# Kernel optimization log

Measured on AMD Instinct MI355X. Metric: run time of the kernel, lower is better.

The kernel has to match this reference:

```python
import jax, jax.numpy as jnp
import numpy as np

EPS_BN = 1e-5
EPS_LN = 1e-5


def conv2d(x, w, stride=1, padding=0):
    # x: [B,C,H,W], w: [O,I,kh,kw]
    return jax.lax.conv_general_dilated(
        x, w, (stride, stride), [(padding, padding), (padding, padding)],
        dimension_numbers=("NCHW", "OIHW", "NCHW"))


def bn_relu(x, g, b, m, v):
    inv = g / jnp.sqrt(v + EPS_BN)
    return jax.nn.relu(x * inv[None, :, None, None] + (b - m * inv)[None, :, None, None])


def haar_dwt(x):
    # orthonormal 2D Haar: [B,C,H,W] -> [B,4C,H/2,W/2] as concat(LL,LH,HL,HH)
    B, C, H, W = x.shape
    x = x.reshape(B, C, H // 2, 2, W // 2, 2)
    a = x[:, :, :, 0, :, 0]; b = x[:, :, :, 0, :, 1]
    c = x[:, :, :, 1, :, 0]; d = x[:, :, :, 1, :, 1]
    ll = (a + b + c + d) * 0.5
    lh = (a - b + c - d) * 0.5
    hl = (a + b - c - d) * 0.5
    hh = (a - b - c + d) * 0.5
    return jnp.concatenate([ll, lh, hl, hh], axis=1)


def haar_idwt(co):
    # exact inverse of haar_dwt: [B,4C,h,w] -> [B,C,2h,2w]
    B, C4, h, w = co.shape
    ll, lh, hl, hh = jnp.split(co, 4, axis=1)
    a = (ll + lh + hl + hh) * 0.5
    b = (ll - lh + hl - hh) * 0.5
    c = (ll + lh - hl - hh) * 0.5
    d = (ll - lh - hl + hh) * 0.5
    row0 = jnp.stack([a, b], axis=-1)  # [B,C,h,w,2]
    row1 = jnp.stack([c, d], axis=-1)
    y = jnp.stack([row0, row1], axis=3)  # [B,C,h,2,w,2]
    return y.reshape(B, C4 // 4, 2 * h, 2 * w)


def layernorm(x, g, b):
    mu = jnp.mean(x, axis=-1, keepdims=True)
    var = jnp.mean(jnp.square(x - mu), axis=-1, keepdims=True)
    return (x - mu) * jax.lax.rsqrt(var + EPS_LN) * g + b


def setup_inputs() -> dict:
    key = jax.random.key(0)
    ks = jax.random.split(key, 20)
    B, N, C = 16, 3136, 256
    red = C // 4  # 64
    sr = 2
    d = {}
    d["x"] = jax.random.normal(ks[0], (B, N, C), jnp.float32)
    d["height"] = 56
    d["width"] = 56
    # reduce: conv1x1 C->red (no bias) + BN
    d["reduce_w"] = jax.random.normal(ks[1], (red, C, 1, 1), jnp.float32) * 0.05
    d["bn1_g"] = jax.random.uniform(ks[2], (red,), jnp.float32, 0.5, 1.5)
    d["bn1_b"] = jax.random.normal(ks[3], (red,), jnp.float32) * 0.1
    d["bn1_m"] = jax.random.normal(ks[4], (red,), jnp.float32) * 0.1
    d["bn1_v"] = jax.random.uniform(ks[5], (red,), jnp.float32, 0.5, 1.5)
    # filter: conv3x3 C->C (no bias) + BN  (acts on 4*red = C coeff channels)
    d["filt_w"] = jax.random.normal(ks[6], (C, C, 3, 3), jnp.float32) * 0.02
    d["bn2_g"] = jax.random.uniform(ks[7], (C,), jnp.float32, 0.5, 1.5)
    d["bn2_b"] = jax.random.normal(ks[8], (C,), jnp.float32) * 0.1
    d["bn2_m"] = jax.random.normal(ks[9], (C,), jnp.float32) * 0.1
    d["bn2_v"] = jax.random.uniform(ks[10], (C,), jnp.float32, 0.5, 1.5)
    # kv_embed: conv kxk stride sr, C->C, with bias
    d["kve_w"] = jax.random.normal(ks[11], (C, C, sr, sr), jnp.float32) * 0.05
    d["kve_b"] = jnp.zeros((C,), jnp.float32)
    # q linear
    d["q_w"] = jax.random.normal(ks[12], (C, C), jnp.float32) * 0.05
    d["q_b"] = jnp.zeros((C,), jnp.float32)
    # kv layernorm + kv linear
    d["kvn_g"] = jnp.ones((C,), jnp.float32)
    d["kvn_b"] = jnp.zeros((C,), jnp.float32)
    d["kv_w"] = jax.random.normal(ks[13], (2 * C, C), jnp.float32) * 0.05
    d["kv_b"] = jnp.zeros((2 * C,), jnp.float32)
    # proj: (C + red) -> C
    d["proj_w"] = jax.random.normal(ks[14], (C, C + red), jnp.float32) * 0.05
    d["proj_b"] = jnp.zeros((C,), jnp.float32)
    return d


def reference(x, q_w, q_b, reduce_w, bn1_g, bn1_b, bn1_m, bn1_v,
              filt_w, bn2_g, bn2_b, bn2_m, bn2_v, kve_w, kve_b,
              kvn_g, kvn_b, kv_w, kv_b, proj_w, proj_b, height, width):
    B, N, C = x.shape
    H_heads, sr = 8, 2
    hd = C // H_heads
    scale = hd ** -0.5

    # queries [B,h,N,hd]
    q = (x @ q_w.T + q_b).reshape(B, N, H_heads, hd).transpose(0, 2, 1, 3)

    # spatial path
    spatial = x.transpose(0, 2, 1).reshape(B, C, height, width)
    reduced = bn_relu(conv2d(spatial, reduce_w), bn1_g, bn1_b, bn1_m, bn1_v)  # [B,C/4,H,W]
    coeffs = haar_dwt(reduced)  # [B,C,H/2,W/2]
    coeffs = bn_relu(conv2d(coeffs, filt_w, padding=1), bn2_g, bn2_b, bn2_m, bn2_v)
    local_context = haar_idwt(coeffs)  # [B,C/4,H,W]
    local_context = local_context.reshape(B, C // 4, N).transpose(0, 2, 1)  # [B,N,C/4]

    # kv path
    kv_src = conv2d(coeffs, kve_w, stride=sr) + kve_b[None, :, None, None]
    Bk, Ck, hk, wk = kv_src.shape
    kv_src = kv_src.reshape(B, C, hk * wk).transpose(0, 2, 1)  # [B,M,C]
    kv_src = layernorm(kv_src, kvn_g, kvn_b)
    kv = (kv_src @ kv_w.T + kv_b).reshape(B, -1, 2, H_heads, hd)
    kv = kv.transpose(2, 0, 3, 1, 4)  # [2,B,h,M,hd]
    key, value = kv[0], kv[1]

    # attention
    scores = jnp.einsum("bhnd,bhmd->bhnm", q, key) * scale
    probs = jax.nn.softmax(scores, axis=-1)
    attended = jnp.einsum("bhnm,bhmd->bhnd", probs, value)
    attended = attended.transpose(0, 2, 1, 3).reshape(B, N, C)

    out = jnp.concatenate([attended, local_context], axis=-1) @ proj_w.T + proj_b
    return out
```

## Files before the change

### kernel.cpp

```cpp
#include <hip/hip_runtime.h>
#include <hip/hip_bf16.h>
#include <math.h>


#define B_   16
#define NSP  3136
#define KVL  196
#define HD   32
#define LSTR 40

typedef short bf16x8 __attribute__((ext_vector_type(8)));
typedef float f32x4  __attribute__((ext_vector_type(4)));

__device__ inline unsigned int f2bf(float f) {
    unsigned int u = __float_as_uint(f);
    u += 0x7FFFu + ((u >> 16) & 1u);
    return u >> 16;
}
__device__ inline float bf2f(unsigned short u) {
    return __uint_as_float(((unsigned int)u) << 16);
}
__device__ inline f32x4 max4(f32x4 a, f32x4 b) {
    f32x4 r;
    r[0] = fmaxf(a[0], b[0]); r[1] = fmaxf(a[1], b[1]);
    r[2] = fmaxf(a[2], b[2]); r[3] = fmaxf(a[3], b[3]);
    return r;
}

__global__ __launch_bounds__(256) void wall_k(
    const float* __restrict__ q, const float* __restrict__ red,
    const float* __restrict__ kv, const float* __restrict__ proj,
    const float* __restrict__ kve, const float* __restrict__ filt,
    unsigned short* __restrict__ wpl, unsigned short* __restrict__ wkve,
    unsigned short* __restrict__ wfilt)
{
    const int bid = blockIdx.x;
    if (bid < 288) {
        const int i = bid * 256 + threadIdx.x;
        const int e = i * 4;
        const float* src; int off;
        if (e < 65536)       { src = q;    off = e; }
        else if (e < 81920)  { src = red;  off = e - 65536; }
        else if (e < 212992) { src = kv;   off = e - 81920; }
        else                 { src = proj; off = e - 212992; }
        const float4 v = *(const float4*)(src + off);
        const unsigned int p0 = f2bf(v.x) | (f2bf(v.y) << 16);
        const unsigned int p1 = f2bf(v.z) | (f2bf(v.w) << 16);
        *(uint2*)(wpl + e) = make_uint2(p0, p1);
    } else if (bid < 544) {
        const int i = (bid - 288) * 256 + threadIdx.x;
        const int n = i >> 8;
        const int rem = i & 255;
        const int tap = rem >> 6;
        const int ci0 = (rem & 63) * 4;
        const float* s = kve + (size_t)n * 1024;
        const unsigned int t0 = f2bf(s[(ci0 + 0) * 4 + tap]);
        const unsigned int t1 = f2bf(s[(ci0 + 1) * 4 + tap]);
        const unsigned int t2 = f2bf(s[(ci0 + 2) * 4 + tap]);
        const unsigned int t3 = f2bf(s[(ci0 + 3) * 4 + tap]);
        *(uint2*)(wkve + (size_t)n * 1024 + tap * 256 + ci0) =
            make_uint2(t0 | (t1 << 16), t2 | (t3 << 16));
    } else {
        const int i = (bid - 544) * 256 + threadIdx.x;
        const int n = i / 576;
        const int rem = (i - n * 576) * 4;
        const int tap = rem >> 8;
        const int ci = rem & 255;
        const float* s = filt + (size_t)n * 2304;
        const unsigned int t0 = f2bf(s[(ci + 0) * 9 + tap]);
        const unsigned int t1 = f2bf(s[(ci + 1) * 9 + tap]);
        const unsigned int t2 = f2bf(s[(ci + 2) * 9 + tap]);
        const unsigned int t3 = f2bf(s[(ci + 3) * 9 + tap]);
        *(uint2*)(wfilt + (size_t)n * 2304 + rem) =
            make_uint2(t0 | (t1 << 16), t2 | (t3 << 16));
    }
}

template<int BM, int BN, int EPI, int LDM>
__global__ __launch_bounds__(256) void mgemm(
    const unsigned short* __restrict__ A, const float* __restrict__ Af,
    const unsigned short* __restrict__ Acl,
    const unsigned short* __restrict__ W, const float* __restrict__ bias,
    const float* __restrict__ g, const float* __restrict__ bb,
    const float* __restrict__ mm, const float* __restrict__ vv,
    float* __restrict__ out, float* __restrict__ out2,
    int Mpad, int Mvalid, int N, int K, float scale)
{
    constexpr int FM = BM / 32, FN = BN / 32;
    constexpr int RA = BM / 64, RB = BN / 64;
    __shared__ short As[BM][LSTR];
    __shared__ short Bs[BN][LSTR];
    const int tid = threadIdx.x, lane = tid & 63;
    const int w = tid >> 6, wr = w >> 1, wc = w & 1;
    const int b = blockIdx.z, m0 = blockIdx.x * BM, n0 = blockIdx.y * BN;
    const unsigned short* Ab = A + ((size_t)b * Mpad + m0) * (size_t)K;
    const unsigned short* Wb = W + (size_t)n0 * K;

    const int r_row0 = tid >> 2, kbase = (tid & 3) * 8;
    int ym[RA], xm[RA], mg[RA];
#pragma unroll
    for (int rnd = 0; rnd < RA; ++rnd) {
        const int m = m0 + rnd * 64 + r_row0;
        mg[rnd] = m;
        if constexpr (LDM == 1) { ym[rnd] = m / 28; xm[rnd] = m - 28 * ym[rnd]; }
        else if constexpr (LDM == 3) { ym[rnd] = m / 14; xm[rnd] = m - 14 * ym[rnd]; }
        else { ym[rnd] = 0; xm[rnd] = 0; }
    }

    f32x4 acc[FM][FN];
#pragma unroll
    for (int i = 0; i < FM; ++i)
#pragma unroll
        for (int j = 0; j < FN; ++j) acc[i][j] = (f32x4){0.f, 0.f, 0.f, 0.f};

    for (int k0 = 0; k0 < K; k0 += 32) {
#pragma unroll
        for (int rnd = 0; rnd < RA; ++rnd) {
            const int row = rnd * 64 + r_row0;
            if constexpr (LDM == 0) {
                *(int4*)&As[row][kbase] =
                    *(const int4*)(Ab + (size_t)row * K + k0 + kbase);
            } else if constexpr (LDM == 2) {
                unsigned int p0 = 0, p1 = 0, p2 = 0, p3 = 0;
                if (mg[rnd] < Mvalid) {
                    const float* sp = Af + ((size_t)b * Mvalid + mg[rnd]) * K + k0 + kbase;
                    const float4 v0 = *(const float4*)sp;
                    const float4 v1 = *(const float4*)(sp + 4);
                    p0 = f2bf(v0.x) | (f2bf(v0.y) << 16);
                    p1 = f2bf(v0.z) | (f2bf(v0.w) << 16);
                    p2 = f2bf(v1.x) | (f2bf(v1.y) << 16);
                    p3 = f2bf(v1.z) | (f2bf(v1.w) << 16);
                }
                *(int4*)&As[row][kbase] = make_int4(p0, p1, p2, p3);
            } else if constexpr (LDM == 1) {
                const int kk = k0 + kbase;
                const int tap = kk >> 8, ci0 = kk & 255;
                const int ky = tap / 3, kx = tap - 3 * ky;
                const int sy = ym[rnd] + ky - 1, sx = xm[rnd] + kx - 1;
                int4 v = make_int4(0, 0, 0, 0);
                if (mg[rnd] < Mvalid && sy >= 0 && sy < 28 && sx >= 0 && sx < 28)
                    v = *(const int4*)(Acl + ((size_t)b * 784 + sy * 28 + sx) * 256 + ci0);
                *(int4*)&As[row][kbase] = v;
            } else {
                const int kk = k0 + kbase;
                const int tap = kk >> 8, ci0 = kk & 255;
                const int ky = tap >> 1, kx = tap & 1;
                const int sy = 2 * ym[rnd] + ky, sx = 2 * xm[rnd] + kx;
                int4 v = make_int4(0, 0, 0, 0);
                if (mg[rnd] < Mvalid)
                    v = *(const int4*)(Acl + ((size_t)b * 784 + sy * 28 + sx) * 256 + ci0);
                *(int4*)&As[row][kbase] = v;
            }
        }
#pragma unroll
        for (int rnd = 0; rnd < RB; ++rnd) {
            const int row = rnd * 64 + r_row0;
            *(int4*)&Bs[row][kbase] =
                *(const int4*)(Wb + (size_t)row * K + k0 + kbase);
        }
        __syncthreads();
        bf16x8 af[FM], bfr[FN];
#pragma unroll
        for (int i = 0; i < FM; ++i)
            af[i] = *(const bf16x8*)&As[wr * (BM / 2) + i * 16 + (lane & 15)][(lane >> 4) * 8];
#pragma unroll
        for (int j = 0; j < FN; ++j)
            bfr[j] = *(const bf16x8*)&Bs[wc * (BN / 2) + j * 16 + (lane & 15)][(lane >> 4) * 8];
#pragma unroll
        for (int i = 0; i < FM; ++i)
#pragma unroll
            for (int j = 0; j < FN; ++j)
                acc[i][j] = __builtin_amdgcn_mfma_f32_16x16x32_bf16(af[i], bfr[j], acc[i][j], 0, 0, 0);
        __syncthreads();
    }

    const int cl = lane & 15, rh = lane >> 4;
#pragma unroll
    for (int i = 0; i < FM; ++i) {
#pragma unroll
        for (int j = 0; j < FN; ++j) {
            const int n = n0 + wc * (BN / 2) + j * 16 + cl;
#pragma unroll
            for (int r = 0; r < 4; ++r) {
                const int m = m0 + wr * (BM / 2) + i * 16 + rh * 4 + r;
                if (m >= Mvalid) continue;
                const float v = acc[i][j][r];
                if constexpr (EPI == 0) {
                    out[((size_t)b * Mvalid + m) * N + n] = v + bias[n];
                } else if constexpr (EPI == 1) {
                    unsigned short* qp = (unsigned short*)out;
                    const int h = (n >> 5) & 7, d = n & 31;
                    qp[(((size_t)b * 8 + h) * 3136 + m) * 32 + d] =
                        (unsigned short)f2bf((v + bias[n]) * scale);
                } else if constexpr (EPI == 3) {
                    const float val = v + bias[n];
                    const int h = (n >> 5) & 7, d = n & 31;
                    if (n < 256)
                        ((unsigned short*)out)[(((size_t)b * 8 + h) * 224 + m) * 32 + d] =
                            (unsigned short)f2bf(val);
                    else
                        ((unsigned short*)out2)[(((size_t)b * 8 + h) * 32 + d) * 224 + m] =
                            (unsigned short)f2bf(val);
                } else {
                    const float inv = g[n] * rsqrtf(vv[n] + 1e-5f);
                    const float rr = v * inv + (bb[n] - mm[n] * inv);
                    ((unsigned short*)out)[((size_t)b * Mvalid + m) * N + n] =
                        (unsigned short)f2bf(rr > 0.f ? rr : 0.f);
                }
            }
        }
    }
}

__global__ __launch_bounds__(256) void dwt_k(const unsigned short* __restrict__ rd,
                                             unsigned short* __restrict__ ccl)
{
    const int i = blockIdx.x * 256 + threadIdx.x;
    const int c4 = (i & 15) * 4;
    const int p = i >> 4;
    const int x = p % 28, y = (p / 28) % 28, b = p / 784;
    const unsigned short* ip = rd + ((size_t)b * 3136 + (2 * y) * 56 + 2 * x) * 64 + c4;
    const uint2 u00 = *(const uint2*)(ip);
    const uint2 u01 = *(const uint2*)(ip + 64);
    const uint2 u10 = *(const uint2*)(ip + 56 * 64);
    const uint2 u11 = *(const uint2*)(ip + 57 * 64);
    const unsigned short* s00 = (const unsigned short*)&u00;
    const unsigned short* s01 = (const unsigned short*)&u01;
    const unsigned short* s10 = (const unsigned short*)&u10;
    const unsigned short* s11 = (const unsigned short*)&u11;
    unsigned short ll[4], lh[4], hl[4], hh[4];
#pragma unroll
    for (int j = 0; j < 4; ++j) {
        const float a = bf2f(s00[j]), bq = bf2f(s01[j]);
        const float c = bf2f(s10[j]), d = bf2f(s11[j]);
        ll[j] = (unsigned short)f2bf((a + bq + c + d) * 0.5f);
        lh[j] = (unsigned short)f2bf((a - bq + c - d) * 0.5f);
        hl[j] = (unsigned short)f2bf((a + bq - c - d) * 0.5f);
        hh[j] = (unsigned short)f2bf((a - bq - c + d) * 0.5f);
    }
    unsigned short* op = ccl + ((size_t)b * 784 + y * 28 + x) * 256 + c4;
    *(uint2*)(op)       = make_uint2(ll[0] | (ll[1] << 16), ll[2] | (ll[3] << 16));
    *(uint2*)(op + 64)  = make_uint2(lh[0] | (lh[1] << 16), lh[2] | (lh[3] << 16));
    *(uint2*)(op + 128) = make_uint2(hl[0] | (hl[1] << 16), hl[2] | (hl[3] << 16));
    *(uint2*)(op + 192) = make_uint2(hh[0] | (hh[1] << 16), hh[2] | (hh[3] << 16));
}

__global__ __launch_bounds__(256) void idwt_k(const unsigned short* __restrict__ c2,
                                              unsigned short* __restrict__ aproj)
{
    const int i = blockIdx.x * 256 + threadIdx.x;
    const int c4 = (i & 15) * 4;
    const int p = i >> 4;
    const int m = p % 3136, b = p / 3136;
    const int Y = m / 56, X = m - 56 * Y;
    const int y = Y >> 1, x = X >> 1;
    const unsigned short* ip = c2 + ((size_t)b * 784 + y * 28 + x) * 256 + c4;
    const uint2 ull = *(const uint2*)(ip);
    const uint2 ulh = *(const uint2*)(ip + 64);
    const uint2 uhl = *(const uint2*)(ip + 128);
    const uint2 uhh = *(const uint2*)(ip + 192);
    const unsigned short* sll = (const unsigned short*)&ull;
    const unsigned short* slh = (const unsigned short*)&ulh;
    const unsigned short* shl = (const unsigned short*)&uhl;
    const unsigned short* shh = (const unsigned short*)&uhh;
    const float flh = (X & 1) ? -0.5f : 0.5f;
    const float fhl = (Y & 1) ? -0.5f : 0.5f;
    const float fhh = ((X ^ Y) & 1) ? -0.5f : 0.5f;
    unsigned short o[4];
#pragma unroll
    for (int j = 0; j < 4; ++j) {
        const float v = 0.5f * bf2f(sll[j]) + flh * bf2f(slh[j]) +
                        fhl * bf2f(shl[j]) + fhh * bf2f(shh[j]);
        o[j] = (unsigned short)f2bf(v);
    }
    *(uint2*)(aproj + ((size_t)b * 3200 + m) * 320 + 256 + c4) =
        make_uint2(o[0] | (o[1] << 16), o[2] | (o[3] << 16));
}

__global__ __launch_bounds__(256) void ln_k(const float* __restrict__ in,
                                            const float* __restrict__ g,
                                            const float* __restrict__ bb,
                                            unsigned short* __restrict__ outp)
{
    const int rg = blockIdx.x;
    const int rl = rg & 255, b = rg >> 8;
    const int t = threadIdx.x;
    unsigned short* op = outp + (size_t)rg * 256 + t;
    if (rl >= 196) { *op = 0; return; }
    const float x = in[((size_t)(b * 196) + rl) * 256 + t];
    __shared__ float r1[4], r2[4];
    float s = x;
#pragma unroll
    for (int o = 32; o > 0; o >>= 1) s += __shfl_down(s, o);
    if ((t & 63) == 0) r1[t >> 6] = s;
    __syncthreads();
    const float mu = (r1[0] + r1[1] + r1[2] + r1[3]) * (1.f / 256.f);
    const float d = x - mu;
    float s2 = d * d;
#pragma unroll
    for (int o = 32; o > 0; o >>= 1) s2 += __shfl_down(s2, o);
    if ((t & 63) == 0) r2[t >> 6] = s2;
    __syncthreads();
    const float var = (r2[0] + r2[1] + r2[2] + r2[3]) * (1.f / 256.f);
    *op = (unsigned short)f2bf(d * rsqrtf(var + 1e-5f) * g[t] + bb[t]);
}

__global__ __launch_bounds__(256, 4) void attn_m(
    const unsigned short* __restrict__ qb, const unsigned short* __restrict__ kb,
    const unsigned short* __restrict__ vt, unsigned short* __restrict__ aproj)
{
    __shared__ short Pl[4][16][232];
    const int tid = threadIdx.x, lane = tid & 63, w = tid >> 6;
    const int bh = blockIdx.y, b = bh >> 3, h = bh & 7;
    const int q0w = blockIdx.x * 128 + w * 32;
    if (q0w >= NSP) return;
    const int cl = lane & 15, hi = lane >> 4;
    const unsigned short* kp = kb + (size_t)bh * 224 * 32;
    const unsigned short* vp0 = vt + ((size_t)bh * 32 + cl) * 224;
    const unsigned short* vp1 = vp0 + 16 * 224;
    short* prow = &Pl[w][cl][0];
    float* ol = (float*)&Pl[w][0][0];
    bf16x8 onesf;
#pragma unroll
    for (int j = 0; j < 8; ++j) onesf[j] = (short)0x3F80;
    const int row = lane >> 2, c8 = (lane & 3) * 8;

#pragma unroll
    for (int g = 0; g < 2; ++g) {
        const int q0 = q0w + g * 16;
        const bf16x8 qf = *(const bf16x8*)(qb + ((size_t)bh * 3136 + q0 + cl) * 32 + hi * 8);

        f32x4 s[13];
#pragma unroll
        for (int t = 0; t < 13; ++t) {
            const bf16x8 kf = *(const bf16x8*)(kp + (size_t)(t * 16 + cl) * 32 + hi * 8);
            s[t] = __builtin_amdgcn_mfma_f32_16x16x32_bf16(kf, qf,
                                                           (f32x4){0.f, 0.f, 0.f, 0.f}, 0, 0, 0);
        }
        if (hi) s[12] = (f32x4){-1e30f, -1e30f, -1e30f, -1e30f};

        f32x4 t0 = max4(s[0], s[1]), t1 = max4(s[2], s[3]), t2 = max4(s[4], s[5]);
        f32x4 t3 = max4(s[6], s[7]), t4 = max4(s[8], s[9]), t5 = max4(s[10], s[11]);
        t0 = max4(t0, t1); t2 = max4(t2, t3); t4 = max4(t4, s[12]);
        t0 = max4(t0, t2); t0 = max4(t0, max4(t4, t5));
        float m = fmaxf(fmaxf(t0[0], t0[1]), fmaxf(t0[2], t0[3]));
        m = fmaxf(m, __shfl_xor(m, 16));
        m = fmaxf(m, __shfl_xor(m, 32));

#pragma unroll
        for (int t = 0; t < 13; ++t) {
#pragma unroll
            for (int r = 0; r < 4; ++r)
                s[t][r] = __builtin_amdgcn_exp2f(s[t][r] - m);
        }

#pragma unroll
        for (int t = 0; t < 13; ++t) {
            __hip_bfloat162 pa = __float22bfloat162_rn(make_float2(s[t][0], s[t][1]));
            __hip_bfloat162 pb = __float22bfloat162_rn(make_float2(s[t][2], s[t][3]));
            unsigned int ua, ub;
            __builtin_memcpy(&ua, &pa, 4);
            __builtin_memcpy(&ub, &pb, 4);
            *(uint2*)(prow + t * 16 + hi * 4) = make_uint2(ua, ub);
        }
        *(uint2*)(prow + 208 + hi * 4) = make_uint2(0u, 0u);

        f32x4 o0 = (f32x4){0.f, 0.f, 0.f, 0.f};
        f32x4 o1 = (f32x4){0.f, 0.f, 0.f, 0.f};
        f32x4 osum = (f32x4){0.f, 0.f, 0.f, 0.f};
#pragma unroll
        for (int kk = 0; kk < 7; ++kk) {
            const bf16x8 pf = *(const bf16x8*)(prow + kk * 32 + hi * 8);
            const bf16x8 v0 = *(const bf16x8*)(vp0 + kk * 32 + hi * 8);
            const bf16x8 v1 = *(const bf16x8*)(vp1 + kk * 32 + hi * 8);
            o0 = __builtin_amdgcn_mfma_f32_16x16x32_bf16(pf, v0, o0, 0, 0, 0);
            o1 = __builtin_amdgcn_mfma_f32_16x16x32_bf16(pf, v1, o1, 0, 0, 0);
            osum = __builtin_amdgcn_mfma_f32_16x16x32_bf16(pf, onesf, osum, 0, 0, 0);
        }

#pragma unroll
        for (int r = 0; r < 4; ++r) {
            const float rq = __builtin_amdgcn_rcpf(osum[r]);
            ol[(hi * 4 + r) * 36 + cl]      = o0[r] * rq;
            ol[(hi * 4 + r) * 36 + cl + 16] = o1[r] * rq;
        }
        const float4 b0 = *(const float4*)(ol + row * 36 + c8);
        const float4 b1 = *(const float4*)(ol + row * 36 + c8 + 4);
        __hip_bfloat162 pa = __float22bfloat162_rn(make_float2(b0.x, b0.y));
        __hip_bfloat162 pb = __float22bfloat162_rn(make_float2(b0.z, b0.w));
        __hip_bfloat162 pc = __float22bfloat162_rn(make_float2(b1.x, b1.y));
        __hip_bfloat162 pd = __float22bfloat162_rn(make_float2(b1.z, b1.w));
        unsigned int k0, k1, k2, k3;
        __builtin_memcpy(&k0, &pa, 4);
        __builtin_memcpy(&k1, &pb, 4);
        __builtin_memcpy(&k2, &pc, 4);
        __builtin_memcpy(&k3, &pd, 4);
        *(uint4*)(aproj + ((size_t)b * 3200 + q0 + row) * 320 + h * 32 + c8) =
            make_uint4(k0, k1, k2, k3);
    }
}

extern "C" void kernel_launch(void* const* d_in, const int* in_sizes, int n_in,
                              void* d_out, int out_size, void* d_ws, size_t ws_size,
                              hipStream_t stream)
{
    const float* x        = (const float*)d_in[0];
    const float* reduce_w = (const float*)d_in[3];
    const float* bn1_g    = (const float*)d_in[4];
    const float* bn1_b    = (const float*)d_in[5];
    const float* bn1_m    = (const float*)d_in[6];
    const float* bn1_v    = (const float*)d_in[7];
    const float* filt_w   = (const float*)d_in[8];
    const float* bn2_g    = (const float*)d_in[9];
    const float* bn2_b    = (const float*)d_in[10];
    const float* bn2_m    = (const float*)d_in[11];
    const float* bn2_v    = (const float*)d_in[12];
    const float* kve_w    = (const float*)d_in[13];
    const float* kve_b    = (const float*)d_in[14];
    const float* q_w      = (const float*)d_in[15];
    const float* q_b      = (const float*)d_in[16];
    const float* kvn_g    = (const float*)d_in[17];
    const float* kvn_b    = (const float*)d_in[18];
    const float* kv_w     = (const float*)d_in[19];
    const float* kv_b     = (const float*)d_in[20];
    const float* proj_w   = (const float*)d_in[21];
    const float* proj_b   = (const float*)d_in[22];

    float* out = (float*)d_out;
    float* ws  = (float*)d_ws;

    unsigned short* aproj = (unsigned short*)ws;
    unsigned short* rd_cl = (unsigned short*)(ws +  8192000);
    unsigned short* ccl   = (unsigned short*)(ws +  9797632);
    unsigned short* ccl2  = (unsigned short*)(ws + 11403264);
    float* kv_src         = ws + 13008896;
    unsigned short* kbuf  = (unsigned short*)(ws + 13811712);
    unsigned short* vtb   = (unsigned short*)(ws + 14270464);
    unsigned short* kv_ln = (unsigned short*)(ws + 14729216);
    unsigned short* wpl   = (unsigned short*)(ws + 15253504);
    unsigned short* wkve  = (unsigned short*)(ws + 15400960);
    unsigned short* wfilt = (unsigned short*)(ws + 15532032);
    unsigned short* wq    = wpl;
    unsigned short* wred  = wpl + 65536;
    unsigned short* wkv   = wpl + 81920;
    unsigned short* wproj = wpl + 212992;
    unsigned short* qb    = (unsigned short*)d_out;

    const float scale = 0.17677669529663689f * 1.4426950408889634f;

    wall_k<<<1120, 256, 0, stream>>>(q_w, reduce_w, kv_w, proj_w, kve_w, filt_w,
                                     wpl, wkve, wfilt);

    mgemm<64, 128, 1, 2><<<dim3(49, 2, B_), 256, 0, stream>>>(
        nullptr, x, nullptr, wq, q_b, nullptr, nullptr, nullptr, nullptr,
        out, nullptr, 3136, 3136, 256, 256, scale);

    mgemm<64, 64, 4, 2><<<dim3(49, 1, B_), 256, 0, stream>>>(
        nullptr, x, nullptr, wred, nullptr, bn1_g, bn1_b, bn1_m, bn1_v,
        (float*)rd_cl, nullptr, 3136, 3136, 64, 256, 0.f);

    dwt_k<<<784, 256, 0, stream>>>(rd_cl, ccl);

    mgemm<64, 64, 4, 1><<<dim3(13, 4, B_), 256, 0, stream>>>(
        nullptr, nullptr, ccl, wfilt, nullptr, bn2_g, bn2_b, bn2_m, bn2_v,
        (float*)ccl2, nullptr, 832, 784, 256, 2304, 0.f);

    idwt_k<<<3136, 256, 0, stream>>>(ccl2, aproj);

    mgemm<64, 64, 0, 3><<<dim3(4, 4, B_), 256, 0, stream>>>(
        nullptr, nullptr, ccl2, wkve, kve_b, nullptr, nullptr, nullptr, nullptr,
        kv_src, nullptr, 256, 196, 256, 1024, 0.f);

    ln_k<<<4096, 256, 0, stream>>>(kv_src, kvn_g, kvn_b, kv_ln);

    mgemm<64, 128, 3, 0><<<dim3(4, 4, B_), 256, 0, stream>>>(
        kv_ln, nullptr, nullptr, wkv, kv_b, nullptr, nullptr, nullptr, nullptr,
        (float*)kbuf, (float*)vtb, 256, 196, 512, 256, 0.f);

    attn_m<<<dim3(25, 128), 256, 0, stream>>>(qb, kbuf, vtb, aproj);

    mgemm<64, 128, 0, 0><<<dim3(49, 2, B_), 256, 0, stream>>>(
        aproj, nullptr, nullptr, wproj, proj_b, nullptr, nullptr, nullptr, nullptr,
        out, nullptr, 3200, 3136, 256, 320, 0.f);
}
```

Baseline: 229.5 us.

## Register-prefetch next K tile and XOR-swizzle shared memory in mgemm

The GEMM main loop now loads the next K-slice of A and B from global memory into registers while the MFMAs consume the current slice from LDS. Global latency can then overlap compute instead of stalling before each barrier. The padded LDS rows (stride 40) are replaced by unpadded 32-wide rows with an XOR swizzle on the 8-element slot, to avoid bank conflicts while cutting LDS footprint. The cost is more live registers for the prefetch buffers, which may lower occupancy.

```diff
diff --git a/kernel.cpp b/kernel.cpp
--- a/kernel.cpp
+++ b/kernel.cpp
@@ -7,7 +7,6 @@
 #define NSP  3136
 #define KVL  196
 #define HD   32
-#define LSTR 40
 
 typedef short bf16x8 __attribute__((ext_vector_type(8)));
 typedef float f32x4  __attribute__((ext_vector_type(4)));
@@ -88,8 +87,8 @@
 {
     constexpr int FM = BM / 32, FN = BN / 32;
     constexpr int RA = BM / 64, RB = BN / 64;
-    __shared__ short As[BM][LSTR];
-    __shared__ short Bs[BN][LSTR];
+    __shared__ short As[BM][32];
+    __shared__ short Bs[BN][32];
     const int tid = threadIdx.x, lane = tid & 63;
     const int w = tid >> 6, wr = w >> 1, wc = w & 1;
     const int b = blockIdx.z, m0 = blockIdx.x * BM, n0 = blockIdx.y * BN;
@@ -97,6 +96,10 @@
     const unsigned short* Wb = W + (size_t)n0 * K;
 
     const int r_row0 = tid >> 2, kbase = (tid & 3) * 8;
+    const int wslot = (((tid & 3) ^ ((tid >> 3) & 3))) * 8;
+    const int cl = lane & 15, hi = lane >> 4;
+    const int rslot = ((hi ^ ((cl >> 1) & 3))) * 8;
+
     int ym[RA], xm[RA], mg[RA];
 #pragma unroll
     for (int rnd = 0; rnd < RA; ++rnd) {
@@ -107,19 +110,11 @@
         else { ym[rnd] = 0; xm[rnd] = 0; }
     }
 
-    f32x4 acc[FM][FN];
-#pragma unroll
-    for (int i = 0; i < FM; ++i)
-#pragma unroll
-        for (int j = 0; j < FN; ++j) acc[i][j] = (f32x4){0.f, 0.f, 0.f, 0.f};
-
-    for (int k0 = 0; k0 < K; k0 += 32) {
+    auto loadA = [&](int4* r, int k0) {
 #pragma unroll
         for (int rnd = 0; rnd < RA; ++rnd) {
-            const int row = rnd * 64 + r_row0;
             if constexpr (LDM == 0) {
-                *(int4*)&As[row][kbase] =
-                    *(const int4*)(Ab + (size_t)row * K + k0 + kbase);
+                r[rnd] = *(const int4*)(Ab + (size_t)(rnd * 64 + r_row0) * K + k0 + kbase);
             } else if constexpr (LDM == 2) {
                 unsigned int p0 = 0, p1 = 0, p2 = 0, p3 = 0;
                 if (mg[rnd] < Mvalid) {
@@ -131,7 +126,7 @@
                     p2 = f2bf(v1.x) | (f2bf(v1.y) << 16);
                     p3 = f2bf(v1.z) | (f2bf(v1.w) << 16);
                 }
-                *(int4*)&As[row][kbase] = make_int4(p0, p1, p2, p3);
+                r[rnd] = make_int4(p0, p1, p2, p3);
             } else if constexpr (LDM == 1) {
                 const int kk = k0 + kbase;
                 const int tap = kk >> 8, ci0 = kk & 255;
@@ -140,7 +135,7 @@
                 int4 v = make_int4(0, 0, 0, 0);
                 if (mg[rnd] < Mvalid && sy >= 0 && sy < 28 && sx >= 0 && sx < 28)
                     v = *(const int4*)(Acl + ((size_t)b * 784 + sy * 28 + sx) * 256 + ci0);
-                *(int4*)&As[row][kbase] = v;
+                r[rnd] = v;
             } else {
                 const int kk = k0 + kbase;
                 const int tap = kk >> 8, ci0 = kk & 255;
@@ -149,23 +144,45 @@
                 int4 v = make_int4(0, 0, 0, 0);
                 if (mg[rnd] < Mvalid)
                     v = *(const int4*)(Acl + ((size_t)b * 784 + sy * 28 + sx) * 256 + ci0);
-                *(int4*)&As[row][kbase] = v;
+                r[rnd] = v;
             }
         }
-#pragma unroll
-        for (int rnd = 0; rnd < RB; ++rnd) {
-            const int row = rnd * 64 + r_row0;
-            *(int4*)&Bs[row][kbase] =
-                *(const int4*)(Wb + (size_t)row * K + k0 + kbase);
-        }
+    };
+    auto loadB = [&](int4* r, int k0) {
+#pragma unroll
+        for (int rnd = 0; rnd < RB; ++rnd)
+            r[rnd] = *(const int4*)(Wb + (size_t)(rnd * 64 + r_row0) * K + k0 + kbase);
+    };
+
+    f32x4 acc[FM][FN];
+#pragma unroll
+    for (int i = 0; i < FM; ++i)
+#pragma unroll
+        for (int j = 0; j < FN; ++j) acc[i][j] = (f32x4){0.f, 0.f, 0.f, 0.f};
+
+    int4 rA[RA], rB[RB];
+    loadA(rA, 0);
+    loadB(rB, 0);
+
+    for (int k0 = 0; k0 < K; k0 += 32) {
+#pragma unroll
+        for (int rnd = 0; rnd < RA; ++rnd)
+            *(int4*)&As[rnd * 64 + r_row0][wslot] = rA[rnd];
+#pragma unroll
+        for (int rnd = 0; rnd < RB; ++rnd)
+            *(int4*)&Bs[rnd * 64 + r_row0][wslot] = rB[rnd];
         __syncthreads();
+        if (k0 + 32 < K) {
+            loadA(rA, k0 + 32);
+            loadB(rB, k0 + 32);
+        }
         bf16x8 af[FM], bfr[FN];
 #pragma unroll
         for (int i = 0; i < FM; ++i)
-            af[i] = *(const bf16x8*)&As[wr * (BM / 2) + i * 16 + (lane & 15)][(lane >> 4) * 8];
+            af[i] = *(const bf16x8*)&As[wr * (BM / 2) + i * 16 + cl][rslot];
 #pragma unroll
         for (int j = 0; j < FN; ++j)
-            bfr[j] = *(const bf16x8*)&Bs[wc * (BN / 2) + j * 16 + (lane & 15)][(lane >> 4) * 8];
+            bfr[j] = *(const bf16x8*)&Bs[wc * (BN / 2) + j * 16 + cl][rslot];
 #pragma unroll
         for (int i = 0; i < FM; ++i)
 #pragma unroll
@@ -174,7 +191,7 @@
         __syncthreads();
     }
 
-    const int cl = lane & 15, rh = lane >> 4;
+    const int rh = hi;
 #pragma unroll
     for (int i = 0; i < FM; ++i) {
 #pragma unroll
```

After: 251.6 us. 9.6% more time.
